# Kernel tuning notes

Hardware: AMD Instinct MI355X
Metric: run time of the kernel (lower is better)

## Reference

```python
import jax, jax.numpy as jnp
import numpy as np
from jax.ops import segment_sum, segment_max

N, E, F_IN, H1, H2, HEADS, OUT, G = 50000, 800000, 64, 64, 64, 4, 32, 500

def setup_inputs() -> dict:
    key = jax.random.key(0)
    ks = jax.random.split(key, 12)
    x = jax.random.normal(ks[0], (N, F_IN), dtype=jnp.float32)
    edge_index = jax.random.randint(ks[1], (2, E), 0, N, dtype=jnp.int64)
    batch = jnp.sort(jax.random.randint(ks[2], (N,), 0, G, dtype=jnp.int64))
    def glorot(k, shape):
        fan = shape[0] + shape[-1]
        return jax.random.uniform(k, shape, jnp.float32, -1.0, 1.0) * jnp.sqrt(6.0 / fan)
    return {
        "x": x,
        "edge_index": edge_index,
        "batch": batch,
        "gcn_W": glorot(ks[3], (F_IN, H1)),
        "gcn_b": jnp.zeros((H1,), jnp.float32),
        "gat_W": glorot(ks[4], (H1, HEADS * H2)),
        "att_src": glorot(ks[5], (HEADS, H2)),
        "att_dst": glorot(ks[6], (HEADS, H2)),
        "gat_b": jnp.zeros((HEADS * H2,), jnp.float32),
        "out_W": glorot(ks[7], (HEADS * H2, OUT)),
        "out_b": jnp.zeros((OUT,), jnp.float32),
    }

def reference(x, edge_index, batch, gcn_W, gcn_b, gat_W, att_src, att_dst, gat_b, out_W, out_b):
    n = x.shape[0]
    loop = jnp.arange(n)
    # edges with self-loops: src (j) -> dst (i), PyG convention
    src = jnp.concatenate([edge_index[0], loop])
    dst = jnp.concatenate([edge_index[1], loop])

    # ---- GCNConv: symmetric normalized scatter-add ----
    h = x @ gcn_W                                            # [N, H1]
    deg = segment_sum(jnp.ones_like(dst, dtype=h.dtype), dst, num_segments=n)
    dinv = jnp.where(deg > 0, jax.lax.rsqrt(deg), 0.0)       # deg^{-1/2}
    norm = dinv[src] * dinv[dst]                             # [E']
    h = segment_sum(norm[:, None] * h[src], dst, num_segments=n) + gcn_b
    h = jax.nn.relu(h)

    # ---- GATConv: per-edge attention + segment softmax over dst ----
    g = (h @ gat_W).reshape(n, HEADS, H2)                    # [N, H, C]
    a_s = jnp.einsum('nhc,hc->nh', g, att_src)               # [N, H]
    a_d = jnp.einsum('nhc,hc->nh', g, att_dst)
    e = jax.nn.leaky_relu(a_s[src] + a_d[dst], 0.2)          # [E', H]
    m = segment_max(e, dst, num_segments=n)                  # every node has a self-loop
    e = jnp.exp(e - m[dst])
    denom = segment_sum(e, dst, num_segments=n)
    alpha = e / denom[dst]                                   # [E', H]
    agg = segment_sum(alpha[:, :, None] * g[src], dst, num_segments=n)  # [N, H, C]
    z = jax.nn.relu(agg.reshape(n, HEADS * H2) + gat_b)

    # ---- global mean pool over graphs + output linear ----
    cnt = segment_sum(jnp.ones((n,), z.dtype), batch, num_segments=G)
    pooled = segment_sum(z, batch, num_segments=G) / jnp.maximum(cnt, 1.0)[:, None]
    return pooled @ out_W + out_b
```

## Files before the change

### kernel.cpp

```cpp
#include <hip/hip_runtime.h>
#include <math.h>

#define NN 50000
#define NE 800000
#define NEP (NE + NN)
#define NGRAPH 500
#define NOUT 32
#define NBLK 196

typedef _Float16 half4 __attribute__((ext_vector_type(4)));


__global__ void k_count(const int* __restrict__ dst, int* __restrict__ cnt,
                        int* __restrict__ pos) {
    int e = blockIdx.x * blockDim.x + threadIdx.x;
    if (e < NE) pos[e] = atomicAdd(&cnt[dst[e]], 1);
}

__global__ __launch_bounds__(256) void k_scan1(const int* __restrict__ cnt, int* __restrict__ bsum,
                                               float* __restrict__ pool, float* __restrict__ cnt_g) {
    __shared__ int buf[256];
    int gid = blockIdx.x * 256 + threadIdx.x;
    int v = (gid < NN) ? (cnt[gid] + 1) : 0;
    buf[threadIdx.x] = v;
    for (int j = gid; j < NGRAPH * 256; j += NBLK * 256) pool[j] = 0.f;
    if (gid < NGRAPH) cnt_g[gid] = 0.f;
    __syncthreads();
    for (int off = 128; off; off >>= 1) {
        if (threadIdx.x < off) buf[threadIdx.x] += buf[threadIdx.x + off];
        __syncthreads();
    }
    if (threadIdx.x == 0) bsum[blockIdx.x] = buf[0];
}

__global__ __launch_bounds__(256) void k_scan3(const int* __restrict__ cnt,
                                               const int* __restrict__ bsum,
                                               int* __restrict__ row_ptr,
                                               float* __restrict__ dinv,
                                               int* __restrict__ col) {
    __shared__ int sb[256];
    __shared__ int buf[256];
    int tid = threadIdx.x;
    int bv = (tid < NBLK) ? bsum[tid] : 0;
    sb[tid] = bv;
    __syncthreads();
    for (int off = 1; off < 256; off <<= 1) {
        int t = (tid >= off) ? sb[tid - off] : 0;
        __syncthreads();
        sb[tid] += t;
        __syncthreads();
    }
    int blockoff = (blockIdx.x == 0) ? 0 : sb[blockIdx.x - 1];
    int i = blockIdx.x * 256 + tid;
    int v = (i < NN) ? (cnt[i] + 1) : 0;
    buf[tid] = v;
    __syncthreads();
    for (int off = 1; off < 256; off <<= 1) {
        int t = (tid >= off) ? buf[tid - off] : 0;
        __syncthreads();
        buf[tid] += t;
        __syncthreads();
    }
    if (i < NN) {
        int rp = blockoff + buf[tid] - v;
        row_ptr[i] = rp;
        dinv[i] = rsqrtf((float)(cnt[i] + 1));
        col[rp] = i;
    }
    if (i == 0) row_ptr[NN] = NEP;
}

__global__ void k_fill(const int* __restrict__ src, const int* __restrict__ dst,
                       const int* __restrict__ row_ptr, const int* __restrict__ pos,
                       int* __restrict__ col) {
    int idx = blockIdx.x * blockDim.x + threadIdx.x;
    if (idx < NE) {
        int d = dst[idx];
        col[row_ptr[d] + 1 + pos[idx]] = src[idx];
    }
}


__global__ __launch_bounds__(256) void k_gemm64(const float* __restrict__ A,
                                                const float* __restrict__ B,
                                                _Float16* __restrict__ C16, int n) {
    __shared__ float Bs[64 * 64];
    __shared__ float As[64 * 68];
    int tid = threadIdx.x;
    int rb = blockIdx.x * 64;
    for (int i = tid; i < 1024; i += 256) ((float4*)Bs)[i] = ((const float4*)B)[i];
    for (int i = tid; i < 1024; i += 256) {
        int r = i >> 4, c = i & 15;
        int row = rb + r; if (row >= n) row = n - 1;
        ((float4*)As)[r * 17 + c] = ((const float4*)A)[(size_t)row * 16 + c];
    }
    __syncthreads();
    int lane = tid & 63, wv = tid >> 6;
    int fl = lane & 15, sub = lane >> 4;
    int r0 = wv * 16 + sub * 4;
    const float4* Bs4 = (const float4*)Bs;
    float4 acc0 = {0,0,0,0}, acc1 = {0,0,0,0}, acc2 = {0,0,0,0}, acc3 = {0,0,0,0};
#pragma unroll 4
    for (int k = 0; k < 64; ++k) {
        float4 b4 = Bs4[k * 16 + fl];
        float a0 = As[(r0 + 0) * 68 + k];
        float a1 = As[(r0 + 1) * 68 + k];
        float a2 = As[(r0 + 2) * 68 + k];
        float a3 = As[(r0 + 3) * 68 + k];
        acc0.x += a0 * b4.x; acc0.y += a0 * b4.y; acc0.z += a0 * b4.z; acc0.w += a0 * b4.w;
        acc1.x += a1 * b4.x; acc1.y += a1 * b4.y; acc1.z += a1 * b4.z; acc1.w += a1 * b4.w;
        acc2.x += a2 * b4.x; acc2.y += a2 * b4.y; acc2.z += a2 * b4.z; acc2.w += a2 * b4.w;
        acc3.x += a3 * b4.x; acc3.y += a3 * b4.y; acc3.z += a3 * b4.z; acc3.w += a3 * b4.w;
    }
    int row = rb + r0;
    half4 h0, h1, h2, h3;
    h0.x=(_Float16)acc0.x; h0.y=(_Float16)acc0.y; h0.z=(_Float16)acc0.z; h0.w=(_Float16)acc0.w;
    h1.x=(_Float16)acc1.x; h1.y=(_Float16)acc1.y; h1.z=(_Float16)acc1.z; h1.w=(_Float16)acc1.w;
    h2.x=(_Float16)acc2.x; h2.y=(_Float16)acc2.y; h2.z=(_Float16)acc2.z; h2.w=(_Float16)acc2.w;
    h3.x=(_Float16)acc3.x; h3.y=(_Float16)acc3.y; h3.z=(_Float16)acc3.z; h3.w=(_Float16)acc3.w;
    if (row + 0 < n) ((half4*)(C16 + (size_t)(row + 0) * 64))[fl] = h0;
    if (row + 1 < n) ((half4*)(C16 + (size_t)(row + 1) * 64))[fl] = h1;
    if (row + 2 < n) ((half4*)(C16 + (size_t)(row + 2) * 64))[fl] = h2;
    if (row + 3 < n) ((half4*)(C16 + (size_t)(row + 3) * 64))[fl] = h3;
}

__global__ __launch_bounds__(256) void k_gemm256(const _Float16* __restrict__ A16,
                                                 const float* __restrict__ B,
                                                 const float* __restrict__ att_src,
                                                 const float* __restrict__ att_dst,
                                                 _Float16* __restrict__ g16,
                                                 float* __restrict__ a_s,
                                                 float* __restrict__ a_d) {
    __shared__ float Bs[64 * 256];
    __shared__ float As[32 * 64];
    int tid = threadIdx.x;
    int rb = blockIdx.x * 32;
    for (int i = tid; i < 4096; i += 256) ((float4*)Bs)[i] = ((const float4*)B)[i];
    for (int i = tid; i < 512; i += 256) {
        int r = i >> 4, c = i & 15;
        int row = rb + r; if (row >= NN) row = NN - 1;
        half4 hv = ((const half4*)A16)[(size_t)row * 16 + c];
        float4 f;
        f.x = (float)hv.x; f.y = (float)hv.y; f.z = (float)hv.z; f.w = (float)hv.w;
        ((float4*)As)[i] = f;
    }
    __syncthreads();
    int lane = tid & 63, wv = tid >> 6;
    const float4* Bs4 = (const float4*)Bs;
    float4 as4 = ((const float4*)att_src)[lane];
    float4 ad4 = ((const float4*)att_dst)[lane];
    const float* Aw = As + (wv * 8) * 64;
    float4 acc[8];
#pragma unroll
    for (int r = 0; r < 8; ++r) acc[r] = make_float4(0.f, 0.f, 0.f, 0.f);
#pragma unroll 4
    for (int k = 0; k < 64; ++k) {
        float4 b4 = Bs4[k * 64 + lane];
#pragma unroll
        for (int r = 0; r < 8; ++r) {
            float av = Aw[r * 64 + k];
            acc[r].x += av * b4.x; acc[r].y += av * b4.y;
            acc[r].z += av * b4.z; acc[r].w += av * b4.w;
        }
    }
#pragma unroll
    for (int r = 0; r < 8; ++r) {
        int row = rb + wv * 8 + r;
        bool valid = row < NN;
        if (valid) {
            half4 hv;
            hv.x = (_Float16)acc[r].x; hv.y = (_Float16)acc[r].y;
            hv.z = (_Float16)acc[r].z; hv.w = (_Float16)acc[r].w;
            ((half4*)(g16 + (size_t)row * 256))[lane] = hv;
        }
        float vs = acc[r].x * as4.x + acc[r].y * as4.y + acc[r].z * as4.z + acc[r].w * as4.w;
        float vd = acc[r].x * ad4.x + acc[r].y * ad4.y + acc[r].z * ad4.z + acc[r].w * ad4.w;
#pragma unroll
        for (int off = 1; off < 16; off <<= 1) {
            vs += __shfl_xor(vs, off);
            vd += __shfl_xor(vd, off);
        }
        if (valid && (lane & 15) == 0) {
            a_s[row * 4 + (lane >> 4)] = vs;
            a_d[row * 4 + (lane >> 4)] = vd;
        }
    }
}


__global__ __launch_bounds__(256) void k_gcn_agg(const _Float16* __restrict__ hx16,
                                                 const int* __restrict__ row_ptr,
                                                 const int* __restrict__ col,
                                                 const float* __restrict__ dinv,
                                                 const float* __restrict__ bias,
                                                 _Float16* __restrict__ h16) {
    int wid = (blockIdx.x * blockDim.x + threadIdx.x) >> 6;
    int lane = threadIdx.x & 63;
    if (wid >= NN) return;
    int sub = lane >> 4;
    int fl  = lane & 15;
    int s0 = row_ptr[wid], s1 = row_ptr[wid + 1];
    float di = dinv[wid];
    const half4* hx4 = (const half4*)hx16;
    float ax = 0.f, ay = 0.f, az = 0.f, aw = 0.f;
    int k = s0 + sub;
    for (; k + 4 < s1; k += 8) {
        int sA = col[k], sB = col[k + 4];
        float wA = dinv[sA] * di, wB = dinv[sB] * di;
        half4 vA = hx4[(size_t)sA * 16 + fl];
        half4 vB = hx4[(size_t)sB * 16 + fl];
        ax += wA * (float)vA.x + wB * (float)vB.x;
        ay += wA * (float)vA.y + wB * (float)vB.y;
        az += wA * (float)vA.z + wB * (float)vB.z;
        aw += wA * (float)vA.w + wB * (float)vB.w;
    }
    if (k < s1) {
        int s = col[k];
        float w = dinv[s] * di;
        half4 v = hx4[(size_t)s * 16 + fl];
        ax += w * (float)v.x; ay += w * (float)v.y;
        az += w * (float)v.z; aw += w * (float)v.w;
    }
    ax += __shfl_xor(ax, 16); ax += __shfl_xor(ax, 32);
    ay += __shfl_xor(ay, 16); ay += __shfl_xor(ay, 32);
    az += __shfl_xor(az, 16); az += __shfl_xor(az, 32);
    aw += __shfl_xor(aw, 16); aw += __shfl_xor(aw, 32);
    if (sub == 0) {
        float4 bb = ((const float4*)bias)[fl];
        half4 z;
        z.x = (_Float16)fmaxf(ax + bb.x, 0.f);
        z.y = (_Float16)fmaxf(ay + bb.y, 0.f);
        z.z = (_Float16)fmaxf(az + bb.z, 0.f);
        z.w = (_Float16)fmaxf(aw + bb.w, 0.f);
        ((half4*)(h16 + (size_t)wid * 64))[fl] = z;
    }
}


__device__ __forceinline__ float lrelu(float x) { return x > 0.f ? x : 0.2f * x; }

__global__ __launch_bounds__(256) void k_gat(const _Float16* __restrict__ g16,
                                             const float* __restrict__ a_s,
                                             const float* __restrict__ a_d,
                                             const int* __restrict__ row_ptr,
                                             const int* __restrict__ col,
                                             const float* __restrict__ gat_b,
                                             const int* __restrict__ batch,
                                             float* __restrict__ pool,
                                             float* __restrict__ cnt_g) {
    __shared__ float zpool[256];
    __shared__ int bids[4];
    int tid = threadIdx.x;
    int wv = tid >> 6, lane = tid & 63;
    int wid = blockIdx.x * 4 + wv;
    int hh = lane >> 4;

    int s0 = row_ptr[wid], s1 = row_ptr[wid + 1];
    float adsel = a_d[wid * 4 + hh];
    const half4* gv4 = (const half4*)g16;

    float m = -1e30f, t = 0.f;
    float ax = 0.f, ay = 0.f, az = 0.f, aw = 0.f;

    int k = s0;
    for (; k + 7 < s1; k += 8) {
        int i0 = col[k], i1 = col[k + 1], i2 = col[k + 2], i3 = col[k + 3];
        int i4 = col[k + 4], i5 = col[k + 5], i6 = col[k + 6], i7 = col[k + 7];
        float e0 = lrelu(a_s[i0 * 4 + hh] + adsel);
        float e1 = lrelu(a_s[i1 * 4 + hh] + adsel);
        float e2 = lrelu(a_s[i2 * 4 + hh] + adsel);
        float e3 = lrelu(a_s[i3 * 4 + hh] + adsel);
        float e4 = lrelu(a_s[i4 * 4 + hh] + adsel);
        float e5 = lrelu(a_s[i5 * 4 + hh] + adsel);
        float e6 = lrelu(a_s[i6 * 4 + hh] + adsel);
        float e7 = lrelu(a_s[i7 * 4 + hh] + adsel);
        half4 g0 = gv4[(size_t)i0 * 64 + lane];
        half4 g1 = gv4[(size_t)i1 * 64 + lane];
        half4 g2 = gv4[(size_t)i2 * 64 + lane];
        half4 g3 = gv4[(size_t)i3 * 64 + lane];
        half4 g4v = gv4[(size_t)i4 * 64 + lane];
        half4 g5v = gv4[(size_t)i5 * 64 + lane];
        half4 g6 = gv4[(size_t)i6 * 64 + lane];
        half4 g7 = gv4[(size_t)i7 * 64 + lane];
        float mn = fmaxf(fmaxf(fmaxf(e0, e1), fmaxf(e2, e3)),
                         fmaxf(fmaxf(e4, e5), fmaxf(e6, e7)));
        mn = fmaxf(mn, m);
        float c = __expf(m - mn);
        float w0 = __expf(e0 - mn), w1 = __expf(e1 - mn);
        float w2 = __expf(e2 - mn), w3 = __expf(e3 - mn);
        float w4 = __expf(e4 - mn), w5 = __expf(e5 - mn);
        float w6 = __expf(e6 - mn), w7 = __expf(e7 - mn);
        t = t * c + ((w0 + w1) + (w2 + w3)) + ((w4 + w5) + (w6 + w7));
        ax = ax * c + w0 * (float)g0.x + w1 * (float)g1.x + w2 * (float)g2.x + w3 * (float)g3.x
                    + w4 * (float)g4v.x + w5 * (float)g5v.x + w6 * (float)g6.x + w7 * (float)g7.x;
        ay = ay * c + w0 * (float)g0.y + w1 * (float)g1.y + w2 * (float)g2.y + w3 * (float)g3.y
                    + w4 * (float)g4v.y + w5 * (float)g5v.y + w6 * (float)g6.y + w7 * (float)g7.y;
        az = az * c + w0 * (float)g0.z + w1 * (float)g1.z + w2 * (float)g2.z + w3 * (float)g3.z
                    + w4 * (float)g4v.z + w5 * (float)g5v.z + w6 * (float)g6.z + w7 * (float)g7.z;
        aw = aw * c + w0 * (float)g0.w + w1 * (float)g1.w + w2 * (float)g2.w + w3 * (float)g3.w
                    + w4 * (float)g4v.w + w5 * (float)g5v.w + w6 * (float)g6.w + w7 * (float)g7.w;
        m = mn;
    }
    for (; k + 3 < s1; k += 4) {
        int i0 = col[k], i1 = col[k + 1], i2 = col[k + 2], i3 = col[k + 3];
        float e0 = lrelu(a_s[i0 * 4 + hh] + adsel);
        float e1 = lrelu(a_s[i1 * 4 + hh] + adsel);
        float e2 = lrelu(a_s[i2 * 4 + hh] + adsel);
        float e3 = lrelu(a_s[i3 * 4 + hh] + adsel);
        half4 g0 = gv4[(size_t)i0 * 64 + lane];
        half4 g1 = gv4[(size_t)i1 * 64 + lane];
        half4 g2 = gv4[(size_t)i2 * 64 + lane];
        half4 g3 = gv4[(size_t)i3 * 64 + lane];
        float mn = fmaxf(fmaxf(fmaxf(e0, e1), fmaxf(e2, e3)), m);
        float c = __expf(m - mn);
        float w0 = __expf(e0 - mn), w1 = __expf(e1 - mn);
        float w2 = __expf(e2 - mn), w3 = __expf(e3 - mn);
        t = t * c + (w0 + w1) + (w2 + w3);
        ax = ax * c + w0 * (float)g0.x + w1 * (float)g1.x + w2 * (float)g2.x + w3 * (float)g3.x;
        ay = ay * c + w0 * (float)g0.y + w1 * (float)g1.y + w2 * (float)g2.y + w3 * (float)g3.y;
        az = az * c + w0 * (float)g0.z + w1 * (float)g1.z + w2 * (float)g2.z + w3 * (float)g3.z;
        aw = aw * c + w0 * (float)g0.w + w1 * (float)g1.w + w2 * (float)g2.w + w3 * (float)g3.w;
        m = mn;
    }
    for (; k < s1; ++k) {
        int s = col[k];
        float e = lrelu(a_s[s * 4 + hh] + adsel);
        half4 gv = gv4[(size_t)s * 64 + lane];
        float mn = fmaxf(m, e);
        float c = __expf(m - mn);
        float w = __expf(e - mn);
        t = t * c + w;
        ax = ax * c + w * (float)gv.x;
        ay = ay * c + w * (float)gv.y;
        az = az * c + w * (float)gv.z;
        aw = aw * c + w * (float)gv.w;
        m = mn;
    }
    float r = 1.f / t;

    float4 gb = ((const float4*)gat_b)[lane];
    float zx = fmaxf(ax * r + gb.x, 0.f);
    float zy = fmaxf(ay * r + gb.y, 0.f);
    float zz = fmaxf(az * r + gb.z, 0.f);
    float zw = fmaxf(aw * r + gb.w, 0.f);

    int b = batch[wid];
    if (lane == 0) bids[wv] = b;
    zpool[tid] = 0.f;
    __syncthreads();
    bool uni = (bids[0] == bids[1]) && (bids[1] == bids[2]) && (bids[2] == bids[3]);
    if (uni) {
        atomicAdd(&zpool[lane * 4 + 0], zx);
        atomicAdd(&zpool[lane * 4 + 1], zy);
        atomicAdd(&zpool[lane * 4 + 2], zz);
        atomicAdd(&zpool[lane * 4 + 3], zw);
        __syncthreads();
        if (wv == 0) {
            float* p = pool + (size_t)bids[0] * 256;
            atomicAdd(&p[lane * 4 + 0], zpool[lane * 4 + 0]);
            atomicAdd(&p[lane * 4 + 1], zpool[lane * 4 + 1]);
            atomicAdd(&p[lane * 4 + 2], zpool[lane * 4 + 2]);
            atomicAdd(&p[lane * 4 + 3], zpool[lane * 4 + 3]);
        }
        if (tid == 0) atomicAdd(&cnt_g[bids[0]], 4.0f);
    } else {
        __syncthreads();
        float* p = pool + (size_t)b * 256;
        atomicAdd(&p[lane * 4 + 0], zx);
        atomicAdd(&p[lane * 4 + 1], zy);
        atomicAdd(&p[lane * 4 + 2], zz);
        atomicAdd(&p[lane * 4 + 3], zw);
        if (lane == 0) atomicAdd(&cnt_g[b], 1.0f);
    }
}


__global__ void k_out(const float* __restrict__ pool, const float* __restrict__ cnt_g,
                      const float* __restrict__ W, const float* __restrict__ b,
                      float* __restrict__ out) {
    int idx = blockIdx.x * blockDim.x + threadIdx.x;
    if (idx >= NGRAPH * NOUT) return;
    int gg = idx >> 5, o = idx & 31;
    float c = cnt_g[gg];
    c = c > 1.f ? c : 1.f;
    float rinv = 1.f / c;
    const float* p = pool + (size_t)gg * 256;
    float acc = 0.f;
#pragma unroll 8
    for (int f = 0; f < 256; ++f) acc += p[f] * W[f * 32 + o];
    out[idx] = acc * rinv + b[o];
}


extern "C" void kernel_launch(void* const* d_in, const int* in_sizes, int n_in,
                              void* d_out, int out_size, void* d_ws, size_t ws_size,
                              hipStream_t stream) {
    const float* x       = (const float*)d_in[0];
    const int*   eidx    = (const int*)d_in[1];
    const int*   batch   = (const int*)d_in[2];
    const float* gcn_W   = (const float*)d_in[3];
    const float* gcn_b   = (const float*)d_in[4];
    const float* gat_W   = (const float*)d_in[5];
    const float* att_src = (const float*)d_in[6];
    const float* att_dst = (const float*)d_in[7];
    const float* gat_b   = (const float*)d_in[8];
    const float* out_W   = (const float*)d_in[9];
    const float* out_b   = (const float*)d_in[10];
    float* out = (float*)d_out;

    const int* src = eidx;
    const int* dst = eidx + NE;

    size_t off = 0;
    auto carve = [&](size_t bytes) -> char* {
        char* p = (char*)d_ws + off;
        off += (bytes + 255) & ~(size_t)255;
        return p;
    };
    int*      cnt     = (int*)carve(NN * sizeof(int));
    int*      pos     = (int*)carve((size_t)NE * sizeof(int));
    int*      row_ptr = (int*)carve((NN + 1) * sizeof(int));
    int*      bsum    = (int*)carve(256 * sizeof(int));
    int*      colb    = (int*)carve((size_t)NEP * sizeof(int));
    float*    dinv    = (float*)carve(NN * sizeof(float));
    _Float16* hx16    = (_Float16*)carve((size_t)NN * 64 * sizeof(_Float16));
    _Float16* h16     = (_Float16*)carve((size_t)NN * 64 * sizeof(_Float16));
    _Float16* g16     = (_Float16*)carve((size_t)NN * 256 * sizeof(_Float16));
    float*    a_s     = (float*)carve((size_t)NN * 4 * sizeof(float));
    float*    a_d     = (float*)carve((size_t)NN * 4 * sizeof(float));
    float*    pool    = (float*)carve((size_t)NGRAPH * 256 * sizeof(float));
    float*    cnt_g   = (float*)carve(NGRAPH * sizeof(float));

    hipMemsetAsync(cnt, 0, NN * sizeof(int), stream);

    k_count<<<(NE + 255) / 256, 256, 0, stream>>>(dst, cnt, pos);
    k_scan1<<<NBLK, 256, 0, stream>>>(cnt, bsum, pool, cnt_g);
    k_scan3<<<NBLK, 256, 0, stream>>>(cnt, bsum, row_ptr, dinv, colb);
    k_fill<<<(NE + 255) / 256, 256, 0, stream>>>(src, dst, row_ptr, pos, colb);

    k_gemm64<<<(NN + 63) / 64, 256, 0, stream>>>(x, gcn_W, hx16, NN);
    k_gcn_agg<<<(NN * 64 + 255) / 256, 256, 0, stream>>>(hx16, row_ptr, colb, dinv, gcn_b, h16);

    k_gemm256<<<(NN + 31) / 32, 256, 0, stream>>>(h16, gat_W, att_src, att_dst, g16, a_s, a_d);
    k_gat<<<NN / 4, 256, 0, stream>>>(g16, a_s, a_d, row_ptr, colb, gat_b, batch, pool, cnt_g);

    k_out<<<(NGRAPH * NOUT + 255) / 256, 256, 0, stream>>>(pool, cnt_g, out_W, out_b, out);
}
```

Measured before the change: 340.8 us.

## Reassociate GAT: aggregate 64-wide h per head, apply gat_W after aggregation

Attention logits are now computed as h·(W·att), with the folded weights precomputed and applied inside the GCN aggregation kernel, so g = h@W is never materialised before the gather. The softmax aggregation gathers 64-wide fp16 h rows per head instead of 256-wide g rows, and gat_W is applied afterwards in a fused GEMM+bias+ReLU+pooling kernel. The online softmax max is replaced by a global upper bound (max a_s plus a_d through leaky ReLU), which removes the rescaling work. This cuts gather bandwidth about fourfold. The fixed bound could underflow exp when logit spreads are large, and it adds a global max-reduction pass.

```diff
diff --git a/kernel.cpp b/kernel.cpp
--- a/kernel.cpp
+++ b/kernel.cpp
@@ -9,6 +9,18 @@
 #define NBLK 196
 
 typedef _Float16 half4 __attribute__((ext_vector_type(4)));
+typedef _Float16 half2t __attribute__((ext_vector_type(2)));
+
+__device__ __forceinline__ float lrelu(float x) { return x > 0.f ? x : 0.2f * x; }
+
+__device__ __forceinline__ unsigned fkey(float f) {
+    unsigned b = __float_as_uint(f);
+    return (b & 0x80000000u) ? ~b : (b | 0x80000000u);
+}
+__device__ __forceinline__ float funkey(unsigned k) {
+    unsigned b = (k & 0x80000000u) ? (k & 0x7fffffffu) : ~k;
+    return __uint_as_float(b);
+}
 
 
 __global__ void k_count(const int* __restrict__ dst, int* __restrict__ cnt,
@@ -124,67 +136,17 @@
     if (row + 3 < n) ((half4*)(C16 + (size_t)(row + 3) * 64))[fl] = h3;
 }
 
-__global__ __launch_bounds__(256) void k_gemm256(const _Float16* __restrict__ A16,
-                                                 const float* __restrict__ B,
-                                                 const float* __restrict__ att_src,
-                                                 const float* __restrict__ att_dst,
-                                                 _Float16* __restrict__ g16,
-                                                 float* __restrict__ a_s,
-                                                 float* __restrict__ a_d) {
-    __shared__ float Bs[64 * 256];
-    __shared__ float As[32 * 64];
-    int tid = threadIdx.x;
-    int rb = blockIdx.x * 32;
-    for (int i = tid; i < 4096; i += 256) ((float4*)Bs)[i] = ((const float4*)B)[i];
-    for (int i = tid; i < 512; i += 256) {
-        int r = i >> 4, c = i & 15;
-        int row = rb + r; if (row >= NN) row = NN - 1;
-        half4 hv = ((const half4*)A16)[(size_t)row * 16 + c];
-        float4 f;
-        f.x = (float)hv.x; f.y = (float)hv.y; f.z = (float)hv.z; f.w = (float)hv.w;
-        ((float4*)As)[i] = f;
-    }
-    __syncthreads();
-    int lane = tid & 63, wv = tid >> 6;
-    const float4* Bs4 = (const float4*)Bs;
-    float4 as4 = ((const float4*)att_src)[lane];
-    float4 ad4 = ((const float4*)att_dst)[lane];
-    const float* Aw = As + (wv * 8) * 64;
-    float4 acc[8];
-#pragma unroll
-    for (int r = 0; r < 8; ++r) acc[r] = make_float4(0.f, 0.f, 0.f, 0.f);
-#pragma unroll 4
-    for (int k = 0; k < 64; ++k) {
-        float4 b4 = Bs4[k * 64 + lane];
-#pragma unroll
-        for (int r = 0; r < 8; ++r) {
-            float av = Aw[r * 64 + k];
-            acc[r].x += av * b4.x; acc[r].y += av * b4.y;
-            acc[r].z += av * b4.z; acc[r].w += av * b4.w;
-        }
-    }
-#pragma unroll
-    for (int r = 0; r < 8; ++r) {
-        int row = rb + wv * 8 + r;
-        bool valid = row < NN;
-        if (valid) {
-            half4 hv;
-            hv.x = (_Float16)acc[r].x; hv.y = (_Float16)acc[r].y;
-            hv.z = (_Float16)acc[r].z; hv.w = (_Float16)acc[r].w;
-            ((half4*)(g16 + (size_t)row * 256))[lane] = hv;
-        }
-        float vs = acc[r].x * as4.x + acc[r].y * as4.y + acc[r].z * as4.z + acc[r].w * as4.w;
-        float vd = acc[r].x * ad4.x + acc[r].y * ad4.y + acc[r].z * ad4.z + acc[r].w * ad4.w;
-#pragma unroll
-        for (int off = 1; off < 16; off <<= 1) {
-            vs += __shfl_xor(vs, off);
-            vd += __shfl_xor(vd, off);
-        }
-        if (valid && (lane & 15) == 0) {
-            a_s[row * 4 + (lane >> 4)] = vs;
-            a_d[row * 4 + (lane >> 4)] = vd;
-        }
-    }
+
+__global__ void k_uv(const float* __restrict__ gat_W, const float* __restrict__ att_src,
+                     const float* __restrict__ att_dst, float* __restrict__ UV) {
+    int idx = blockIdx.x * blockDim.x + threadIdx.x;
+    if (idx >= 512) return;
+    int f = idx >> 3, o = idx & 7, h = o & 3;
+    const float* av = (o < 4) ? att_src : att_dst;
+    float s = 0.f;
+#pragma unroll 8
+    for (int c = 0; c < 64; ++c) s += gat_W[f * 256 + h * 64 + c] * av[h * 64 + c];
+    UV[idx] = s;
 }
 
 
@@ -193,7 +155,10 @@
                                                  const int* __restrict__ col,
                                                  const float* __restrict__ dinv,
                                                  const float* __restrict__ bias,
-                                                 _Float16* __restrict__ h16) {
+                                                 const float* __restrict__ UV,
+                                                 _Float16* __restrict__ h16,
+                                                 float* __restrict__ a_s,
+                                                 float* __restrict__ a_d) {
     int wid = (blockIdx.x * blockDim.x + threadIdx.x) >> 6;
     int lane = threadIdx.x & 63;
     if (wid >= NN) return;
@@ -225,152 +190,203 @@
     ay += __shfl_xor(ay, 16); ay += __shfl_xor(ay, 32);
     az += __shfl_xor(az, 16); az += __shfl_xor(az, 32);
     aw += __shfl_xor(aw, 16); aw += __shfl_xor(aw, 32);
+    float4 bb = ((const float4*)bias)[fl];
+    float zx = fmaxf(ax + bb.x, 0.f);
+    float zy = fmaxf(ay + bb.y, 0.f);
+    float zz = fmaxf(az + bb.z, 0.f);
+    float zw = fmaxf(aw + bb.w, 0.f);
     if (sub == 0) {
-        float4 bb = ((const float4*)bias)[fl];
         half4 z;
-        z.x = (_Float16)fmaxf(ax + bb.x, 0.f);
-        z.y = (_Float16)fmaxf(ay + bb.y, 0.f);
-        z.z = (_Float16)fmaxf(az + bb.z, 0.f);
-        z.w = (_Float16)fmaxf(aw + bb.w, 0.f);
+        z.x = (_Float16)zx; z.y = (_Float16)zy; z.z = (_Float16)zz; z.w = (_Float16)zw;
         ((half4*)(h16 + (size_t)wid * 64))[fl] = z;
     }
-}
-
-
-__device__ __forceinline__ float lrelu(float x) { return x > 0.f ? x : 0.2f * x; }
-
-__global__ __launch_bounds__(256) void k_gat(const _Float16* __restrict__ g16,
-                                             const float* __restrict__ a_s,
-                                             const float* __restrict__ a_d,
-                                             const int* __restrict__ row_ptr,
-                                             const int* __restrict__ col,
-                                             const float* __restrict__ gat_b,
-                                             const int* __restrict__ batch,
-                                             float* __restrict__ pool,
-                                             float* __restrict__ cnt_g) {
-    __shared__ float zpool[256];
-    __shared__ int bids[4];
+    int f0 = fl * 4;
+    float ps = zx * UV[(f0 + 0) * 8 + sub] + zy * UV[(f0 + 1) * 8 + sub]
+             + zz * UV[(f0 + 2) * 8 + sub] + zw * UV[(f0 + 3) * 8 + sub];
+    float pd = zx * UV[(f0 + 0) * 8 + 4 + sub] + zy * UV[(f0 + 1) * 8 + 4 + sub]
+             + zz * UV[(f0 + 2) * 8 + 4 + sub] + zw * UV[(f0 + 3) * 8 + 4 + sub];
+    ps += __shfl_xor(ps, 1); pd += __shfl_xor(pd, 1);
+    ps += __shfl_xor(ps, 2); pd += __shfl_xor(pd, 2);
+    ps += __shfl_xor(ps, 4); pd += __shfl_xor(pd, 4);
+    ps += __shfl_xor(ps, 8); pd += __shfl_xor(pd, 8);
+    if (fl == 0) {
+        a_s[wid * 4 + sub] = ps;
+        a_d[wid * 4 + sub] = pd;
+    }
+}
+
+
+__global__ __launch_bounds__(256) void k_gmax(const float* __restrict__ a_s,
+                                              unsigned* __restrict__ gmaxU) {
+    __shared__ unsigned sm[4];
+    int tid = threadIdx.x;
+    if (tid < 4) sm[tid] = 0u;
+    __syncthreads();
+    float mx = -1e30f, my = -1e30f, mz = -1e30f, mw = -1e30f;
+    int stride = gridDim.x * 256;
+    for (int n = blockIdx.x * 256 + tid; n < NN; n += stride) {
+        float4 v = ((const float4*)a_s)[n];
+        mx = fmaxf(mx, v.x); my = fmaxf(my, v.y);
+        mz = fmaxf(mz, v.z); mw = fmaxf(mw, v.w);
+    }
+    atomicMax(&sm[0], fkey(mx)); atomicMax(&sm[1], fkey(my));
+    atomicMax(&sm[2], fkey(mz)); atomicMax(&sm[3], fkey(mw));
+    __syncthreads();
+    if (tid < 4) atomicMax(&gmaxU[tid], sm[tid]);
+}
+
+
+__global__ __launch_bounds__(256) void k_gat_h(const _Float16* __restrict__ h16,
+                                               const float* __restrict__ a_s,
+                                               const float* __restrict__ a_d,
+                                               const int* __restrict__ row_ptr,
+                                               const int* __restrict__ col,
+                                               const unsigned* __restrict__ gmaxU,
+                                               _Float16* __restrict__ aggH) {
     int tid = threadIdx.x;
     int wv = tid >> 6, lane = tid & 63;
     int wid = blockIdx.x * 4 + wv;
     int hh = lane >> 4;
+    int fl = lane & 15;
 
     int s0 = row_ptr[wid], s1 = row_ptr[wid + 1];
     float adsel = a_d[wid * 4 + hh];
-    const half4* gv4 = (const half4*)g16;
-
-    float m = -1e30f, t = 0.f;
+    float M = lrelu(funkey(gmaxU[hh]) + adsel);
+    const half4* h4 = (const half4*)h16;
+
+    float t = 1e-30f;
     float ax = 0.f, ay = 0.f, az = 0.f, aw = 0.f;
 
     int k = s0;
     for (; k + 7 < s1; k += 8) {
         int i0 = col[k], i1 = col[k + 1], i2 = col[k + 2], i3 = col[k + 3];
         int i4 = col[k + 4], i5 = col[k + 5], i6 = col[k + 6], i7 = col[k + 7];
-        float e0 = lrelu(a_s[i0 * 4 + hh] + adsel);
-        float e1 = lrelu(a_s[i1 * 4 + hh] + adsel);
-        float e2 = lrelu(a_s[i2 * 4 + hh] + adsel);
-        float e3 = lrelu(a_s[i3 * 4 + hh] + adsel);
-        float e4 = lrelu(a_s[i4 * 4 + hh] + adsel);
-        float e5 = lrelu(a_s[i5 * 4 + hh] + adsel);
-        float e6 = lrelu(a_s[i6 * 4 + hh] + adsel);
-        float e7 = lrelu(a_s[i7 * 4 + hh] + adsel);
-        half4 g0 = gv4[(size_t)i0 * 64 + lane];
-        half4 g1 = gv4[(size_t)i1 * 64 + lane];
-        half4 g2 = gv4[(size_t)i2 * 64 + lane];
-        half4 g3 = gv4[(size_t)i3 * 64 + lane];
-        half4 g4v = gv4[(size_t)i4 * 64 + lane];
-        half4 g5v = gv4[(size_t)i5 * 64 + lane];
-        half4 g6 = gv4[(size_t)i6 * 64 + lane];
-        half4 g7 = gv4[(size_t)i7 * 64 + lane];
-        float mn = fmaxf(fmaxf(fmaxf(e0, e1), fmaxf(e2, e3)),
-                         fmaxf(fmaxf(e4, e5), fmaxf(e6, e7)));
-        mn = fmaxf(mn, m);
-        float c = __expf(m - mn);
-        float w0 = __expf(e0 - mn), w1 = __expf(e1 - mn);
-        float w2 = __expf(e2 - mn), w3 = __expf(e3 - mn);
-        float w4 = __expf(e4 - mn), w5 = __expf(e5 - mn);
-        float w6 = __expf(e6 - mn), w7 = __expf(e7 - mn);
-        t = t * c + ((w0 + w1) + (w2 + w3)) + ((w4 + w5) + (w6 + w7));
-        ax = ax * c + w0 * (float)g0.x + w1 * (float)g1.x + w2 * (float)g2.x + w3 * (float)g3.x
-                    + w4 * (float)g4v.x + w5 * (float)g5v.x + w6 * (float)g6.x + w7 * (float)g7.x;
-        ay = ay * c + w0 * (float)g0.y + w1 * (float)g1.y + w2 * (float)g2.y + w3 * (float)g3.y
-                    + w4 * (float)g4v.y + w5 * (float)g5v.y + w6 * (float)g6.y + w7 * (float)g7.y;
-        az = az * c + w0 * (float)g0.z + w1 * (float)g1.z + w2 * (float)g2.z + w3 * (float)g3.z
-                    + w4 * (float)g4v.z + w5 * (float)g5v.z + w6 * (float)g6.z + w7 * (float)g7.z;
-        aw = aw * c + w0 * (float)g0.w + w1 * (float)g1.w + w2 * (float)g2.w + w3 * (float)g3.w
-                    + w4 * (float)g4v.w + w5 * (float)g5v.w + w6 * (float)g6.w + w7 * (float)g7.w;
-        m = mn;
+        half4 g0 = h4[(size_t)i0 * 16 + fl];
+        half4 g1 = h4[(size_t)i1 * 16 + fl];
+        half4 g2 = h4[(size_t)i2 * 16 + fl];
+        half4 g3 = h4[(size_t)i3 * 16 + fl];
+        half4 g4v = h4[(size_t)i4 * 16 + fl];
+        half4 g5v = h4[(size_t)i5 * 16 + fl];
+        half4 g6 = h4[(size_t)i6 * 16 + fl];
+        half4 g7 = h4[(size_t)i7 * 16 + fl];
+        float w0 = __expf(lrelu(a_s[i0 * 4 + hh] + adsel) - M);
+        float w1 = __expf(lrelu(a_s[i1 * 4 + hh] + adsel) - M);
+        float w2 = __expf(lrelu(a_s[i2 * 4 + hh] + adsel) - M);
+        float w3 = __expf(lrelu(a_s[i3 * 4 + hh] + adsel) - M);
+        float w4 = __expf(lrelu(a_s[i4 * 4 + hh] + adsel) - M);
+        float w5 = __expf(lrelu(a_s[i5 * 4 + hh] + adsel) - M);
+        float w6 = __expf(lrelu(a_s[i6 * 4 + hh] + adsel) - M);
+        float w7 = __expf(lrelu(a_s[i7 * 4 + hh] + adsel) - M);
+        t += ((w0 + w1) + (w2 + w3)) + ((w4 + w5) + (w6 + w7));
+        ax += w0 * (float)g0.x + w1 * (float)g1.x + w2 * (float)g2.x + w3 * (float)g3.x
+            + w4 * (float)g4v.x + w5 * (float)g5v.x + w6 * (float)g6.x + w7 * (float)g7.x;
+        ay += w0 * (float)g0.y + w1 * (float)g1.y + w2 * (float)g2.y + w3 * (float)g3.y
+            + w4 * (float)g4v.y + w5 * (float)g5v.y + w6 * (float)g6.y + w7 * (float)g7.y;
+        az += w0 * (float)g0.z + w1 * (float)g1.z + w2 * (float)g2.z + w3 * (float)g3.z
+            + w4 * (float)g4v.z + w5 * (float)g5v.z + w6 * (float)g6.z + w7 * (float)g7.z;
+        aw += w0 * (float)g0.w + w1 * (float)g1.w + w2 * (float)g2.w + w3 * (float)g3.w
+            + w4 * (float)g4v.w + w5 * (float)g5v.w + w6 * (float)g6.w + w7 * (float)g7.w;
     }
     for (; k + 3 < s1; k += 4) {
         int i0 = col[k], i1 = col[k + 1], i2 = col[k + 2], i3 = col[k + 3];
-        float e0 = lrelu(a_s[i0 * 4 + hh] + adsel);
-        float e1 = lrelu(a_s[i1 * 4 + hh] + adsel);
-        float e2 = lrelu(a_s[i2 * 4 + hh] + adsel);
-        float e3 = lrelu(a_s[i3 * 4 + hh] + adsel);
-        half4 g0 = gv4[(size_t)i0 * 64 + lane];
-        half4 g1 = gv4[(size_t)i1 * 64 + lane];
-        half4 g2 = gv4[(size_t)i2 * 64 + lane];
-        half4 g3 = gv4[(size_t)i3 * 64 + lane];
-        float mn = fmaxf(fmaxf(fmaxf(e0, e1), fmaxf(e2, e3)), m);
-        float c = __expf(m - mn);
-        float w0 = __expf(e0 - mn), w1 = __expf(e1 - mn);
-        float w2 = __expf(e2 - mn), w3 = __expf(e3 - mn);
-        t = t * c + (w0 + w1) + (w2 + w3);
-        ax = ax * c + w0 * (float)g0.x + w1 * (float)g1.x + w2 * (float)g2.x + w3 * (float)g3.x;
-        ay = ay * c + w0 * (float)g0.y + w1 * (float)g1.y + w2 * (float)g2.y + w3 * (float)g3.y;
-        az = az * c + w0 * (float)g0.z + w1 * (float)g1.z + w2 * (float)g2.z + w3 * (float)g3.z;
-        aw = aw * c + w0 * (float)g0.w + w1 * (float)g1.w + w2 * (float)g2.w + w3 * (float)g3.w;
-        m = mn;
+        half4 g0 = h4[(size_t)i0 * 16 + fl];
+        half4 g1 = h4[(size_t)i1 * 16 + fl];
+        half4 g2 = h4[(size_t)i2 * 16 + fl];
+        half4 g3 = h4[(size_t)i3 * 16 + fl];
+        float w0 = __expf(lrelu(a_s[i0 * 4 + hh] + adsel) - M);
+        float w1 = __expf(lrelu(a_s[i1 * 4 + hh] + adsel) - M);
+        float w2 = __expf(lrelu(a_s[i2 * 4 + hh] + adsel) - M);
+        float w3 = __expf(lrelu(a_s[i3 * 4 + hh] + adsel) - M);
+        t += (w0 + w1) + (w2 + w3);
+        ax += w0 * (float)g0.x + w1 * (float)g1.x + w2 * (float)g2.x + w3 * (float)g3.x;
+        ay += w0 * (float)g0.y + w1 * (float)g1.y + w2 * (float)g2.y + w3 * (float)g3.y;
+        az += w0 * (float)g0.z + w1 * (float)g1.z + w2 * (float)g2.z + w3 * (float)g3.z;
+        aw += w0 * (float)g0.w + w1 * (float)g1.w + w2 * (float)g2.w + w3 * (float)g3.w;
     }
     for (; k < s1; ++k) {
         int s = col[k];
-        float e = lrelu(a_s[s * 4 + hh] + adsel);
-        half4 gv = gv4[(size_t)s * 64 + lane];
-        float mn = fmaxf(m, e);
-        float c = __expf(m - mn);
-        float w = __expf(e - mn);
-        t = t * c + w;
-        ax = ax * c + w * (float)gv.x;
-        ay = ay * c + w * (float)gv.y;
-        az = az * c + w * (float)gv.z;
-        aw = aw * c + w * (float)gv.w;
-        m = mn;
+        half4 gv = h4[(size_t)s * 16 + fl];
+        float w = __expf(lrelu(a_s[s * 4 + hh] + adsel) - M);
+        t += w;
+        ax += w * (float)gv.x; ay += w * (float)gv.y;
+        az += w * (float)gv.z; aw += w * (float)gv.w;
     }
     float r = 1.f / t;
-
+    half4 o;
+    o.x = (_Float16)(ax * r); o.y = (_Float16)(ay * r);
+    o.z = (_Float16)(az * r); o.w = (_Float16)(aw * r);
+    ((half4*)(aggH + (size_t)wid * 256))[lane] = o;
+}
+
+
+__global__ __launch_bounds__(256) void k_post(const _Float16* __restrict__ aggH,
+                                              const float* __restrict__ W,
+                                              const float* __restrict__ gat_b,
+                                              const int* __restrict__ batch,
+                                              float* __restrict__ pool,
+                                              float* __restrict__ cnt_g) {
+    __shared__ float Bs[64 * 256];
+    __shared__ _Float16 As[32 * 256];
+    int tid = threadIdx.x;
+    int rb = blockIdx.x * 32;
+    for (int i = tid; i < 4096; i += 256) ((float4*)Bs)[i] = ((const float4*)W)[i];
+    for (int i = tid; i < 1024; i += 256) {
+        int r = i >> 5, c = i & 31;
+        int row = rb + r; if (row >= NN) row = NN - 1;
+        ((float4*)As)[i] = ((const float4*)(aggH + (size_t)row * 256))[c];
+    }
+    __syncthreads();
+    int lane = tid & 63, wv = tid >> 6, hh = lane >> 4;
+    const float4* Bs4 = (const float4*)Bs;
+    const _Float16* Ar = As + (size_t)(wv * 8) * 256 + hh * 64;
+    float4 acc[8];
+#pragma unroll
+    for (int r = 0; r < 8; ++r) acc[r] = make_float4(0.f, 0.f, 0.f, 0.f);
+    for (int k = 0; k < 64; k += 2) {
+        int kr = (k + hh * 16) & 63;
+        float4 b0 = Bs4[kr * 64 + lane];
+        float4 b1 = Bs4[(kr + 1) * 64 + lane];
+#pragma unroll
+        for (int r = 0; r < 8; ++r) {
+            half2t a2 = *(const half2t*)(Ar + r * 256 + kr);
+            float a0 = (float)a2.x, a1 = (float)a2.y;
+            acc[r].x += a0 * b0.x + a1 * b1.x;
+            acc[r].y += a0 * b0.y + a1 * b1.y;
+            acc[r].z += a0 * b0.z + a1 * b1.z;
+            acc[r].w += a0 * b0.w + a1 * b1.w;
+        }
+    }
     float4 gb = ((const float4*)gat_b)[lane];
-    float zx = fmaxf(ax * r + gb.x, 0.f);
-    float zy = fmaxf(ay * r + gb.y, 0.f);
-    float zz = fmaxf(az * r + gb.z, 0.f);
-    float zw = fmaxf(aw * r + gb.w, 0.f);
-
-    int b = batch[wid];
-    if (lane == 0) bids[wv] = b;
-    zpool[tid] = 0.f;
-    __syncthreads();
-    bool uni = (bids[0] == bids[1]) && (bids[1] == bids[2]) && (bids[2] == bids[3]);
-    if (uni) {
-        atomicAdd(&zpool[lane * 4 + 0], zx);
-        atomicAdd(&zpool[lane * 4 + 1], zy);
-        atomicAdd(&zpool[lane * 4 + 2], zz);
-        atomicAdd(&zpool[lane * 4 + 3], zw);
-        __syncthreads();
-        if (wv == 0) {
-            float* p = pool + (size_t)bids[0] * 256;
-            atomicAdd(&p[lane * 4 + 0], zpool[lane * 4 + 0]);
-            atomicAdd(&p[lane * 4 + 1], zpool[lane * 4 + 1]);
-            atomicAdd(&p[lane * 4 + 2], zpool[lane * 4 + 2]);
-            atomicAdd(&p[lane * 4 + 3], zpool[lane * 4 + 3]);
+    int r0 = rb + wv * 8;
+    int iA = r0 < NN ? r0 : NN - 1;
+    int iB = (r0 + 7) < NN ? (r0 + 7) : NN - 1;
+    int bA = batch[iA], bB = batch[iB];
+    if (bA == bB && r0 + 7 < NN) {
+        float sx = 0.f, sy = 0.f, sz = 0.f, sw = 0.f;
+#pragma unroll
+        for (int r = 0; r < 8; ++r) {
+            sx += fmaxf(acc[r].x + gb.x, 0.f);
+            sy += fmaxf(acc[r].y + gb.y, 0.f);
+            sz += fmaxf(acc[r].z + gb.z, 0.f);
+            sw += fmaxf(acc[r].w + gb.w, 0.f);
         }
-        if (tid == 0) atomicAdd(&cnt_g[bids[0]], 4.0f);
+        float* p = pool + (size_t)bA * 256 + lane * 4;
+        atomicAdd(p + 0, sx); atomicAdd(p + 1, sy);
+        atomicAdd(p + 2, sz); atomicAdd(p + 3, sw);
+        if (lane == 0) atomicAdd(&cnt_g[bA], 8.f);
     } else {
-        __syncthreads();
-        float* p = pool + (size_t)b * 256;
-        atomicAdd(&p[lane * 4 + 0], zx);
-        atomicAdd(&p[lane * 4 + 1], zy);
-        atomicAdd(&p[lane * 4 + 2], zz);
-        atomicAdd(&p[lane * 4 + 3], zw);
-        if (lane == 0) atomicAdd(&cnt_g[b], 1.0f);
+        for (int r = 0; r < 8; ++r) {
+            int row = r0 + r;
+            if (row < NN) {
+                int b = batch[row];
+                float* p = pool + (size_t)b * 256 + lane * 4;
+                atomicAdd(p + 0, fmaxf(acc[r].x + gb.x, 0.f));
+                atomicAdd(p + 1, fmaxf(acc[r].y + gb.y, 0.f));
+                atomicAdd(p + 2, fmaxf(acc[r].z + gb.z, 0.f));
+                atomicAdd(p + 3, fmaxf(acc[r].w + gb.w, 0.f));
+                if (lane == 0) atomicAdd(&cnt_g[b], 1.f);
+            }
+        }
     }
 }
 
@@ -425,24 +441,32 @@
     float*    dinv    = (float*)carve(NN * sizeof(float));
     _Float16* hx16    = (_Float16*)carve((size_t)NN * 64 * sizeof(_Float16));
     _Float16* h16     = (_Float16*)carve((size_t)NN * 64 * sizeof(_Float16));
-    _Float16* g16     = (_Float16*)carve((size_t)NN * 256 * sizeof(_Float16));
+    _Float16* aggH16  = (_Float16*)carve((size_t)NN * 256 * sizeof(_Float16));
     float*    a_s     = (float*)carve((size_t)NN * 4 * sizeof(float));
     float*    a_d     = (float*)carve((size_t)NN * 4 * sizeof(float));
+    float*    UV      = (float*)carve(64 * 8 * sizeof(float));
+    unsigned* gmaxU   = (unsigned*)carve(4 * sizeof(unsigned));
     float*    pool    = (float*)carve((size_t)NGRAPH * 256 * sizeof(float));
     float*    cnt_g   = (float*)carve(NGRAPH * sizeof(float));
 
     hipMemsetAsync(cnt, 0, NN * sizeof(int), stream);
+    hipMemsetAsync(gmaxU, 0, 4 * sizeof(unsigned), stream);
 
     k_count<<<(NE + 255) / 256, 256, 0, stream>>>(dst, cnt, pos);
     k_scan1<<<NBLK, 256, 0, stream>>>(cnt, bsum, pool, cnt_g);
     k_scan3<<<NBLK, 256, 0, stream>>>(cnt, bsum, row_ptr, dinv, colb);
     k_fill<<<(NE + 255) / 256, 256, 0, stream>>>(src, dst, row_ptr, pos, colb);
 
+    k_uv<<<2, 256, 0, stream>>>(gat_W, att_src, att_dst, UV);
+
     k_gemm64<<<(NN + 63) / 64, 256, 0, stream>>>(x, gcn_W, hx16, NN);
-    k_gcn_agg<<<(NN * 64 + 255) / 256, 256, 0, stream>>>(hx16, row_ptr, colb, dinv, gcn_b, h16);
-
-    k_gemm256<<<(NN + 31) / 32, 256, 0, stream>>>(h16, gat_W, att_src, att_dst, g16, a_s, a_d);
-    k_gat<<<NN / 4, 256, 0, stream>>>(g16, a_s, a_d, row_ptr, colb, gat_b, batch, pool, cnt_g);
+    k_gcn_agg<<<(NN * 64 + 255) / 256, 256, 0, stream>>>(hx16, row_ptr, colb, dinv, gcn_b,
+                                                         UV, h16, a_s, a_d);
+
+    k_gmax<<<128, 256, 0, stream>>>(a_s, gmaxU);
+    k_gat_h<<<NN / 4, 256, 0, stream>>>(h16, a_s, a_d, row_ptr, colb, gmaxU, aggH16);
+
+    k_post<<<(NN + 31) / 32, 256, 0, stream>>>(aggH16, gat_W, gat_b, batch, pool, cnt_g);
 
     k_out<<<(NGRAPH * NOUT + 255) / 256, 256, 0, stream>>>(pool, cnt_g, out_W, out_b, out);
 }
```

Result: slower. 368.3 us (+8.0%).
